# Performance work log

Hardware: AMD Instinct MI355X
Metric: run time of the kernel (lower is better)

The kernel has to match this reference:

```python
import jax, jax.numpy as jnp
import numpy as np

# (in_ch, out_ch) per conv layer per SA stage (use_xyz adds +3 to first in-ch)
DIMS = {1: [(3, 64), (64, 64), (64, 128)],
        2: [(131, 128), (128, 128), (128, 256)],
        3: [(259, 256), (256, 512), (512, 1024)]}
B, N = 32, 4096


def setup_inputs() -> dict:
    key = jax.random.key(0)
    key, k = jax.random.split(key)
    inp = {"pointcloud": jax.random.uniform(k, (B, N, 3), jnp.float32)}
    for s in (1, 2, 3):
        for l, (ci, co) in enumerate(DIMS[s]):
            key, k1, k2, k3 = jax.random.split(key, 4)
            inp[f"w{s}{l}"] = jax.random.normal(k1, (ci, co), jnp.float32) * (1.0 / np.sqrt(ci))
            # eval-mode BatchNorm folded to per-channel scale g and bias b
            inp[f"g{s}{l}"] = 1.0 + 0.1 * jax.random.normal(k2, (co,), jnp.float32)
            inp[f"b{s}{l}"] = 0.1 * jax.random.normal(k3, (co,), jnp.float32)
    return inp


def fps(xyz, npoint):
    """Farthest point sampling. xyz: (B,N,3) -> idx (B,npoint) int32. First index is 0."""
    n = xyz.shape[1]
    def one(pts):
        def body(carry, _):
            dist, last = carry
            d = jnp.sum((pts - pts[last]) ** 2, axis=-1)
            dist = jnp.minimum(dist, d)
            nxt = jnp.argmax(dist).astype(jnp.int32)
            return (dist, nxt), nxt
        init = (jnp.full((n,), 1e10, pts.dtype), jnp.int32(0))
        _, idxs = jax.lax.scan(body, init, None, length=npoint - 1)
        return jnp.concatenate([jnp.zeros((1,), jnp.int32), idxs])
    return jax.vmap(one)(xyz)


def ball_query(xyz, centers, radius, nsample):
    """xyz (B,N,3), centers (B,S,3) -> idx (B,S,nsample): first nsample in-ball point
    indices, deficits padded with the first found index (matches CUDA ball_query)."""
    n = xyz.shape[1]
    d2 = jnp.sum((centers[:, :, None, :] - xyz[:, None, :, :]) ** 2, axis=-1)  # (B,S,N)
    keyv = jnp.where(d2 < radius * radius, jnp.arange(n)[None, None, :], n)
    sk = jnp.sort(keyv, axis=-1)[..., :nsample]  # ascending valid indices, pad = n
    first = sk[..., :1]
    idx = jnp.where(sk == n, first, sk)
    return jnp.clip(idx, 0, n - 1)


def gather(pts, idx):
    """pts (B,N,C), idx (B,...) -> (B,...,C)"""
    return jax.vmap(lambda p, i: p[i])(pts, idx)


def shared_mlp(x, params):
    """x (..., Cin); each layer: 1x1 conv (matmul) + folded-BN affine + ReLU."""
    for w, g, b in params:
        x = jax.nn.relu(jnp.einsum('...c,cd->...d', x, w) * g + b)
    return x


def sa_module(xyz, feat, npoint, radius, nsample, params):
    ctr_idx = fps(xyz, npoint)
    new_xyz = gather(xyz, ctr_idx)                        # (B,S,3)
    idx = ball_query(xyz, new_xyz, radius, nsample)       # (B,S,K)
    g_xyz = gather(xyz, idx) - new_xyz[:, :, None, :]     # (B,S,K,3) centered
    grouped = g_xyz if feat is None else jnp.concatenate([g_xyz, gather(feat, idx)], axis=-1)
    h = shared_mlp(grouped, params)                       # (B,S,K,Cout)
    return new_xyz, jnp.max(h, axis=2)                    # max-pool over neighbors


def reference(pointcloud, w10, g10, b10, w11, g11, b11, w12, g12, b12,
              w20, g20, b20, w21, g21, b21, w22, g22, b22,
              w30, g30, b30, w31, g31, b31, w32, g32, b32):
    p1 = [(w10, g10, b10), (w11, g11, b11), (w12, g12, b12)]
    p2 = [(w20, g20, b20), (w21, g21, b21), (w22, g22, b22)]
    p3 = [(w30, g30, b30), (w31, g31, b31), (w32, g32, b32)]
    xyz = pointcloud[..., :3]
    xyz, feat = sa_module(xyz, None, 512, 0.2, 64, p1)
    xyz, feat = sa_module(xyz, feat, 128, 0.4, 64, p2)
    # group-all SA: one group containing all points, xyz NOT centered
    grouped = jnp.concatenate([xyz, feat], axis=-1)[:, None]  # (B,1,S,259)
    h = shared_mlp(grouped, p3)                                # (B,1,S,1024)
    return jnp.max(h, axis=2)[:, 0]                            # (B,1024)
```

## Files before the change

### kernel.cpp

```cpp
#include <hip/hip_runtime.h>
#include <math.h>

#define NTH 256

using short8 = __attribute__((ext_vector_type(8))) short;
using f32x4  = __attribute__((ext_vector_type(4))) float;

__device__ __forceinline__ unsigned short f2bf(float x) {
    unsigned u = __float_as_uint(x);
    u += 0x7fff + ((u >> 16) & 1);
    return (unsigned short)(u >> 16);
}
__device__ __forceinline__ float bf2f(unsigned short h) {
    return __uint_as_float(((unsigned)h) << 16);
}

template<int CTRL>
__device__ __forceinline__ unsigned long long dppmax(unsigned long long k) {
    unsigned lo = (unsigned)k, hi = (unsigned)(k >> 32);
    unsigned plo = (unsigned)__builtin_amdgcn_update_dpp(0, (int)lo, CTRL, 0xF, 0xF, true);
    unsigned phi = (unsigned)__builtin_amdgcn_update_dpp(0, (int)hi, CTRL, 0xF, 0xF, true);
    unsigned long long p = ((unsigned long long)phi << 32) | plo;
    return p > k ? p : k;
}

template<int N, int NPOINT, int NTHR, int NPC, bool INIT, bool SPILL>
__device__ __forceinline__ void fps_body(
    const float* __restrict__ xyz, float* __restrict__ out_xyz, int b, int it0,
    float* __restrict__ pts , float* __restrict__ ctr ,
    unsigned long long* __restrict__ wkey ,
    float* __restrict__ sdist, int* __restrict__ slast)
{
    constexpr int PT = N / NTHR;
    constexpr int NW = NTHR / 64;
    const int tid  = threadIdx.x;
    const int lane = tid & 63;
    const int w    = tid >> 6;
    const float* src = xyz + (size_t)b * N * 3;

    __builtin_amdgcn_s_setprio(1);

    for (int e = tid; e < N * 3; e += NTHR) pts[e] = src[e];

    float px[PT], py[PT], pz[PT], dist[PT];
    unsigned klo[PT];
#pragma unroll
    for (int j = 0; j < PT; ++j) {
        int i = j * NTHR + tid;
        px[j] = src[i * 3 + 0]; py[j] = src[i * 3 + 1]; pz[j] = src[i * 3 + 2];
        klo[j] = ~(unsigned)i;
        dist[j] = 1e10f;
    }
    int last = 0;
    if constexpr (!INIT) {
        const float* sd = sdist + (size_t)b * N;
#pragma unroll
        for (int j = 0; j < PT; ++j) dist[j] = sd[j * NTHR + tid];
        last = slast[b];
    } else {
        if (tid == 0) { ctr[0] = src[0]; ctr[1] = src[1]; ctr[2] = src[2]; }
    }
    __syncthreads();

    constexpr int CBEG = INIT ? 1 : 0;
    for (int c = CBEG; c < NPC; ++c) {
        const float lx = pts[last * 3 + 0];
        const float ly = pts[last * 3 + 1];
        const float lz = pts[last * 3 + 2];
        unsigned long long best = 0ull;
#pragma unroll
        for (int j = 0; j < PT; ++j) {
            float dx = px[j] - lx, dy = py[j] - ly, dz = pz[j] - lz;
            float d = __fadd_rn(__fadd_rn(__fmul_rn(dx, dx), __fmul_rn(dy, dy)),
                                __fmul_rn(dz, dz));
            float nd = fminf(dist[j], d);
            dist[j] = nd;
            unsigned long long key =
                ((unsigned long long)__float_as_uint(nd) << 32) | (unsigned long long)klo[j];
            best = (key > best) ? key : best;
        }
        best = dppmax<0xB1>(best);
        best = dppmax<0x4E>(best);
        best = dppmax<0x141>(best);
        best = dppmax<0x140>(best);
        best = dppmax<0x142>(best);
        best = dppmax<0x143>(best);
        const int p = (c & 1) * NW;
        if (lane == 63) wkey[p + w] = best;
        __syncthreads();
        unsigned long long K0[NW];
#pragma unroll
        for (int v = 0; v < NW; ++v) K0[v] = wkey[p + v];
#pragma unroll
        for (int st = NW / 2; st > 0; st >>= 1)
#pragma unroll
            for (int v = 0; v < st; ++v) K0[v] = (K0[v + st] > K0[v]) ? K0[v + st] : K0[v];
        last = (int)(~(unsigned)K0[0]);
        if (tid == 0) {
            ctr[c * 3 + 0] = pts[last * 3 + 0];
            ctr[c * 3 + 1] = pts[last * 3 + 1];
            ctr[c * 3 + 2] = pts[last * 3 + 2];
        }
    }
    __syncthreads();
    if constexpr (SPILL) {
        float* sd = sdist + (size_t)b * N;
#pragma unroll
        for (int j = 0; j < PT; ++j) sd[j * NTHR + tid] = dist[j];
        if (tid == 0) slast[b] = last;
    }
    float* dst = out_xyz + ((size_t)b * NPOINT + (it0 - CBEG)) * 3;
    for (int e = tid; e < NPC * 3; e += NTHR) dst[e] = ctr[e];
    __builtin_amdgcn_s_setprio(0);
}

#define PREP_TOT 813056
__device__ __forceinline__ void prep_body(
    int gid, int stride,
    const float* __restrict__ w0, const float* __restrict__ w1, const float* __restrict__ w2,
    const float* __restrict__ w3, const float* __restrict__ w4, const float* __restrict__ w5,
    const float* __restrict__ w6, const float* __restrict__ w7, const float* __restrict__ w8,
    unsigned short* __restrict__ outw)
{
    const int K_[9]    = {3, 64, 64, 131, 128, 128, 259, 256, 512};
    const int N_[9]    = {64, 64, 128, 128, 128, 256, 256, 512, 1024};
    const int E_[9]    = {2048, 4096, 8192, 20480, 16384, 32768, 73728, 131072, 524288};
    const int base_[9] = {0, 4096, 12288, 28672, 69632, 102400, 167936, 315392, 577536};
    const int PCF_[9]  = {0, 0, 0, 128, 0, 0, 256, 0, 0};
    const float* W_[9] = {w0, w1, w2, w3, w4, w5, w6, w7, w8};
    for (; gid < PREP_TOT; gid += stride) {
        int i = 0, t = gid;
        while (t >= E_[i]) { t -= E_[i]; ++i; }
        const int Nn = N_[i];
        const int k8 = t / (Nn * 8);
        const int rem = t - k8 * Nn * 8;
        const int col = rem >> 3, j = rem & 7;
        const int k = k8 * 8 + j;
        float v = 0.f;
        if (k < K_[i]) {
            int ks = k;
            const int pcf = PCF_[i];
            if (pcf > 0) ks = (k < pcf) ? (k + 3) : (k - pcf);
            v = W_[i][(size_t)ks * Nn + col];
        }
        unsigned short hi = f2bf(v);
        unsigned short lo = f2bf(v - bf2f(hi));
        outw[base_[i] + t] = hi;
        outw[base_[i] + E_[i] + t] = lo;
    }
}

template<int K, int NSUB, int NOFF, int NFULL, int RTILES, int SX, int SY, bool FINAL>
__device__ __forceinline__ void mfma_layer(
    const unsigned short* __restrict__ whi, const unsigned short* __restrict__ wlo,
    const float* __restrict__ gm, const float* __restrict__ bt,
    const unsigned short* __restrict__ Xhi, const unsigned short* __restrict__ Xlo,
    unsigned short* __restrict__ Yhi, unsigned short* __restrict__ Ylo,
    float* outp, int tid)
{
    constexpr int KP  = (K + 31) & ~31;
    constexpr int KC  = KP / 32;
    constexpr int NTW = NSUB / 64;
    static_assert(NSUB % 64 == 0, "col split");
    const int w = tid >> 6, lane = tid & 63;
    const int lr = lane & 15, lg = lane >> 4;
    const int colbase = NOFF + w * (NSUB / 4);

    f32x4 acc[RTILES][NTW];
#pragma unroll
    for (int m = 0; m < RTILES; ++m)
#pragma unroll
        for (int t = 0; t < NTW; ++t) acc[m][t] = f32x4{0.f, 0.f, 0.f, 0.f};

    const unsigned short* xh0 = Xhi + lr * SX + lg * 8;
    const unsigned short* xl0 = Xlo + lr * SX + lg * 8;

    for (int kc = 0; kc < KC; ++kc) {
        const size_t krow = (size_t)(kc * 4 + lg) * NFULL * 8;
        short8 bh[NTW], bl[NTW];
#pragma unroll
        for (int t = 0; t < NTW; ++t) {
            const int col = colbase + t * 16 + lr;
            bh[t] = *reinterpret_cast<const short8*>(whi + krow + (size_t)col * 8);
            bl[t] = *reinterpret_cast<const short8*>(wlo + krow + (size_t)col * 8);
        }
#pragma unroll
        for (int m = 0; m < RTILES; ++m) {
            short8 ah = *reinterpret_cast<const short8*>(xh0 + m * 16 * SX + kc * 32);
            short8 al = *reinterpret_cast<const short8*>(xl0 + m * 16 * SX + kc * 32);
#pragma unroll
            for (int t = 0; t < NTW; ++t) {
                acc[m][t] = __builtin_amdgcn_mfma_f32_16x16x32_bf16(ah, bh[t], acc[m][t], 0, 0, 0);
                acc[m][t] = __builtin_amdgcn_mfma_f32_16x16x32_bf16(ah, bl[t], acc[m][t], 0, 0, 0);
                acc[m][t] = __builtin_amdgcn_mfma_f32_16x16x32_bf16(al, bh[t], acc[m][t], 0, 0, 0);
            }
        }
    }
#pragma unroll
    for (int t = 0; t < NTW; ++t) {
        const int col = colbase + t * 16 + lr;
        const float gv = gm[col], bv = bt[col];
        if constexpr (FINAL) {
            float mx = 0.f;
#pragma unroll
            for (int m = 0; m < RTILES; ++m)
#pragma unroll
                for (int r = 0; r < 4; ++r)
                    mx = fmaxf(mx, fmaxf(fmaf(acc[m][t][r], gv, bv), 0.f));
            mx = fmaxf(mx, __shfl_xor(mx, 16));
            mx = fmaxf(mx, __shfl_xor(mx, 32));
            if (lg == 0)
                atomicMax(reinterpret_cast<int*>(outp) + col, __float_as_int(mx));
        } else {
#pragma unroll
            for (int m = 0; m < RTILES; ++m)
#pragma unroll
                for (int r = 0; r < 4; ++r) {
                    float v = fmaxf(fmaf(acc[m][t][r], gv, bv), 0.f);
                    unsigned short hi = f2bf(v);
                    unsigned short lo = f2bf(v - bf2f(hi));
                    const int row = m * 16 + lg * 4 + r;
                    Yhi[row * SY + col] = hi;
                    Ylo[row * SY + col] = lo;
                }
        }
    }
}

template<int CF, int C0, int C1, int C2, int R>
struct SaCfg {
    static constexpr int CIN = 3 + CF;
    static constexpr int KP0 = (CIN + 31) & ~31;
    static constexpr int SX = KP0 + 8, SY1 = C0 + 8, SY2 = C1 + 8;
    static constexpr int RT = R / 16;
    static constexpr int OFF_Y1 = 0;
    static constexpr int OFF_X = 2 * R * SY1;
    static constexpr int XSZ = 2 * R * SX, Y2SZ = 2 * R * SY2;
    static constexpr int TOT = OFF_X + (XSZ > Y2SZ ? XSZ : Y2SZ);
    static constexpr int BYTES = TOT * 2 + 264 * 4;
};

template<int CF, int C0, int C1, int C2, int R>
__device__ __forceinline__ void sa_body(
    unsigned short* __restrict__ sm, int* __restrict__ bqm,
    int b, int cs, int S, int half,
    const float* __restrict__ src_xyz, const float* __restrict__ src_feat,
    const float* __restrict__ centers,
    const unsigned short* __restrict__ w0h, const unsigned short* __restrict__ w0l,
    const unsigned short* __restrict__ w1h, const unsigned short* __restrict__ w1l,
    const unsigned short* __restrict__ w2h, const unsigned short* __restrict__ w2l,
    const float* __restrict__ g0, const float* __restrict__ b0,
    const float* __restrict__ g1, const float* __restrict__ b1,
    const float* __restrict__ g2, const float* __restrict__ b2,
    float* __restrict__ out_feat, int N, float r2)
{
    using C = SaCfg<CF, C0, C1, C2, R>;
    constexpr int TPR = NTH / R;
    const int tid  = threadIdx.x;
    const int lane = tid & 63;
    const int w    = tid >> 6;
    const int bs   = b * S + cs;

    const float cx = centers[(size_t)bs * 3 + 0];
    const float cy = centers[(size_t)bs * 3 + 1];
    const float cz = centers[(size_t)bs * 3 + 2];

    {
        const int seg = N >> 2;
        const float* px = src_xyz + (size_t)b * N * 3;
        int count = 0, first = -1;
        const int bend = (w + 1) * seg;
        for (int base = w * seg; base < bend && count < 64; base += 64) {
            int i = base + lane;
            float dx = px[i * 3 + 0] - cx, dy = px[i * 3 + 1] - cy, dz = px[i * 3 + 2] - cz;
            float d2 = __fadd_rn(__fadd_rn(__fmul_rn(dx, dx), __fmul_rn(dy, dy)),
                                 __fmul_rn(dz, dz));
            bool inb = d2 < r2;
            unsigned long long m = __ballot(inb);
            if (first < 0 && m) first = base + (__ffsll(m) - 1);
            if (inb) {
                int pos = count + (int)__popcll(m & ((1ull << lane) - 1ull));
                if (pos < 64) bqm[w * 64 + pos] = i;
            }
            count += (int)__popcll(m);
        }
        if (lane == 0) {
            bqm[256 + w] = count > 64 ? 64 : count;
            bqm[260 + w] = first;
        }
    }
    __syncthreads();

    unsigned short* Xhi = sm + C::OFF_X;    unsigned short* Xlo = Xhi + R * C::SX;
    unsigned short* Y1h = sm + C::OFF_Y1;   unsigned short* Y1l = Y1h + R * C::SY1;
    unsigned short* Y2h = sm + C::OFF_X;    unsigned short* Y2l = Y2h + R * C::SY2;

    {
        const int r = tid / TPR, s = tid % TPR;
        int pid;
        {
            const int cA = bqm[256 + 0], cB = bqm[256 + 1], cC = bqm[256 + 2], cD = bqm[256 + 3];
            const int tot = cA + cB + cC + cD;
            int t = half * R + r;
            if (t < tot) {
                int ww = 0;
                if (t >= cA) { t -= cA; ww = 1;
                    if (t >= cB) { t -= cB; ww = 2;
                        if (t >= cC) { t -= cC; ww = 3; } } }
                pid = bqm[ww * 64 + t];
            } else {
                const int fA = bqm[260 + 0], fB = bqm[260 + 1], fC = bqm[260 + 2], fD = bqm[260 + 3];
                pid = fA >= 0 ? fA : (fB >= 0 ? fB : (fC >= 0 ? fC : (fD >= 0 ? fD : (N - 1))));
            }
        }
        unsigned short* xh = Xhi + r * C::SX;
        unsigned short* xl = Xlo + r * C::SX;
        if constexpr (CF > 0) {
            constexpr int CPT = CF / TPR;
            const float* frow = src_feat + ((size_t)b * N + pid) * CF + s * CPT;
#pragma unroll
            for (int q = 0; q < CPT / 4; ++q) {
                float4 v4 = *reinterpret_cast<const float4*>(frow + q * 4);
                ushort4 h, l;
                h.x = f2bf(v4.x); l.x = f2bf(v4.x - bf2f(h.x));
                h.y = f2bf(v4.y); l.y = f2bf(v4.y - bf2f(h.y));
                h.z = f2bf(v4.z); l.z = f2bf(v4.z - bf2f(h.z));
                h.w = f2bf(v4.w); l.w = f2bf(v4.w - bf2f(h.w));
                *reinterpret_cast<ushort4*>(xh + s * CPT + q * 4) = h;
                *reinterpret_cast<ushort4*>(xl + s * CPT + q * 4) = l;
            }
        }
        if (s < 3) {
            float p = src_xyz[((size_t)b * N + pid) * 3 + s]
                      - (s == 0 ? cx : (s == 1 ? cy : cz));
            unsigned short hi = f2bf(p), lo = f2bf(p - bf2f(hi));
            xh[CF + s] = hi; xl[CF + s] = lo;
        }
        constexpr int PADPER = (C::KP0 - C::CIN + TPR - 1) / TPR;
#pragma unroll
        for (int q = 0; q < PADPER; ++q) {
            int c = C::CIN + s * PADPER + q;
            if (c < C::KP0) { xh[c] = 0; xl[c] = 0; }
        }
    }
    __syncthreads();
    mfma_layer<C::CIN, C0, 0, C0, C::RT, C::SX, C::SY1, false>(
        w0h, w0l, g0, b0, Xhi, Xlo, Y1h, Y1l, nullptr, tid);
    __syncthreads();
    mfma_layer<C0, C1, 0, C1, C::RT, C::SY1, C::SY2, false>(
        w1h, w1l, g1, b1, Y1h, Y1l, Y2h, Y2l, nullptr, tid);
    __syncthreads();
    mfma_layer<C1, C2, 0, C2, C::RT, C::SY2, 0, true>(
        w2h, w2l, g2, b2, Y2h, Y2l, nullptr, nullptr,
        out_feat + (size_t)bs * C2, tid);
}

template<int N1>
__global__ __launch_bounds__(NTH) void k_fps1a_prep(
    const float* __restrict__ pc, float* __restrict__ nxyz1,
    const float* __restrict__ w0, const float* __restrict__ w1, const float* __restrict__ w2,
    const float* __restrict__ w3, const float* __restrict__ w4, const float* __restrict__ w5,
    const float* __restrict__ w6, const float* __restrict__ w7, const float* __restrict__ w8,
    unsigned short* __restrict__ outw,
    float* __restrict__ sdist, int* __restrict__ slast,
    float4* __restrict__ z1, int n1, float4* __restrict__ z2, int n2,
    float4* __restrict__ z3, int n3, int nfps, int nprep)
{
    __shared__ float pts[N1 * 3];
    __shared__ float ctr[256 * 3];
    __shared__ unsigned long long wkey[2 * (NTH / 64)];
    if ((int)blockIdx.x < nfps) {
        fps_body<N1, 512, NTH, 256, true, true>(pc, nxyz1, blockIdx.x, 1,
                                                pts, ctr, wkey, sdist, slast);
    } else if ((int)blockIdx.x < nfps + nprep) {
        prep_body((blockIdx.x - nfps) * NTH + threadIdx.x, nprep * NTH,
                  w0, w1, w2, w3, w4, w5, w6, w7, w8, outw);
    } else {
        const int zid = (blockIdx.x - nfps - nprep) * NTH + threadIdx.x;
        const int zs  = (gridDim.x - nfps - nprep) * NTH;
        const float4 zv = make_float4(0.f, 0.f, 0.f, 0.f);
        for (int i = zid; i < n1; i += zs) z1[i] = zv;
        for (int i = zid; i < n2; i += zs) z2[i] = zv;
        for (int i = zid; i < n3; i += zs) z3[i] = zv;
    }
}

__global__ __launch_bounds__(NTH) void k_fps1b2_sa1h1(
    const float* __restrict__ pc, float* __restrict__ nxyz1, float* __restrict__ nxyz2,
    float* __restrict__ sdist, int* __restrict__ slast,
    const unsigned short* __restrict__ w0h, const unsigned short* __restrict__ w0l,
    const unsigned short* __restrict__ w1h, const unsigned short* __restrict__ w1l,
    const unsigned short* __restrict__ w2h, const unsigned short* __restrict__ w2l,
    const float* __restrict__ g0, const float* __restrict__ b0,
    const float* __restrict__ g1, const float* __restrict__ b1,
    const float* __restrict__ g2, const float* __restrict__ b2,
    float* __restrict__ feat1, float r2)
{
    constexpr int FPSB = 4096 * 3 * 4 + 256 * 3 * 4 + 2 * (NTH / 64) * 8;
    constexpr int SAB  = SaCfg<0, 64, 64, 128, 64>::BYTES;
    constexpr int BYTES = FPSB > SAB ? FPSB : SAB;
    __shared__ __align__(16) char raw[BYTES];
    if ((int)blockIdx.x < 32) {
        {
            float* pts = (float*)raw;
            float* ctr = (float*)(raw + 4096 * 3 * 4);
            unsigned long long* wkey = (unsigned long long*)(raw + 4096 * 3 * 4 + 256 * 3 * 4);
            fps_body<4096, 512, NTH, 256, false, false>(pc, nxyz1, blockIdx.x, 256,
                                                        pts, ctr, wkey, sdist, slast);
        }
        __syncthreads();
        {
            float* pts = (float*)raw;
            float* ctr = (float*)(raw + 512 * 3 * 4);
            unsigned long long* wkey = (unsigned long long*)(raw + 512 * 3 * 4 + 128 * 3 * 4);
            fps_body<512, 128, NTH, 128, true, false>(nxyz1, nxyz2, blockIdx.x, 1,
                                                      pts, ctr, wkey, nullptr, nullptr);
        }
    } else {
        const int blk = blockIdx.x - 32;
        const int b = blk >> 8, cs = blk & 255;
        unsigned short* sm = (unsigned short*)raw;
        int* bqm = (int*)(raw + SaCfg<0, 64, 64, 128, 64>::TOT * 2);
        sa_body<0, 64, 64, 128, 64>(sm, bqm, b, cs, 512, 0,
                                    pc, nullptr, nxyz1,
                                    w0h, w0l, w1h, w1l, w2h, w2l,
                                    g0, b0, g1, b1, g2, b2, feat1, 4096, r2);
    }
}

__global__ __launch_bounds__(NTH) void k_sa1h2(
    const float* __restrict__ pc, const float* __restrict__ nxyz1,
    const unsigned short* __restrict__ w0h, const unsigned short* __restrict__ w0l,
    const unsigned short* __restrict__ w1h, const unsigned short* __restrict__ w1l,
    const unsigned short* __restrict__ w2h, const unsigned short* __restrict__ w2l,
    const float* __restrict__ g0, const float* __restrict__ b0,
    const float* __restrict__ g1, const float* __restrict__ b1,
    const float* __restrict__ g2, const float* __restrict__ b2,
    float* __restrict__ feat1, float r2)
{
    using C = SaCfg<0, 64, 64, 128, 64>;
    __shared__ __align__(16) char raw[C::BYTES];
    const int b = blockIdx.x >> 8, cs = 256 + (blockIdx.x & 255);
    unsigned short* sm = (unsigned short*)raw;
    int* bqm = (int*)(raw + C::TOT * 2);
    sa_body<0, 64, 64, 128, 64>(sm, bqm, b, cs, 512, 0,
                                pc, nullptr, nxyz1,
                                w0h, w0l, w1h, w1l, w2h, w2l,
                                g0, b0, g1, b1, g2, b2, feat1, 4096, r2);
}

__global__ __launch_bounds__(NTH) void k_sa2(
    const float* __restrict__ nxyz1, const float* __restrict__ feat1,
    const float* __restrict__ nxyz2,
    const unsigned short* __restrict__ w0h, const unsigned short* __restrict__ w0l,
    const unsigned short* __restrict__ w1h, const unsigned short* __restrict__ w1l,
    const unsigned short* __restrict__ w2h, const unsigned short* __restrict__ w2l,
    const float* __restrict__ g0, const float* __restrict__ b0,
    const float* __restrict__ g1, const float* __restrict__ b1,
    const float* __restrict__ g2, const float* __restrict__ b2,
    float* __restrict__ feat2, float r2)
{
    using C = SaCfg<128, 128, 128, 256, 32>;
    __shared__ __align__(16) char raw[C::BYTES];
    const int half = blockIdx.x & 1;
    const int cb   = blockIdx.x >> 1;
    const int b = cb >> 7, cs = cb & 127;
    unsigned short* sm = (unsigned short*)raw;
    int* bqm = (int*)(raw + C::TOT * 2);
    sa_body<128, 128, 128, 256, 32>(sm, bqm, b, cs, 128, half,
                                    nxyz1, feat1, nxyz2,
                                    w0h, w0l, w1h, w1l, w2h, w2l,
                                    g0, b0, g1, b1, g2, b2, feat2, 512, r2);
}

template<int CF, int C0, int C1, int C2>
__global__ __launch_bounds__(NTH) void head_mfma(
    const float* __restrict__ xyz, const float* __restrict__ feat,
    const unsigned short* __restrict__ w0h, const unsigned short* __restrict__ w0l,
    const unsigned short* __restrict__ w1h, const unsigned short* __restrict__ w1l,
    const unsigned short* __restrict__ w2h, const unsigned short* __restrict__ w2l,
    const float* __restrict__ g0, const float* __restrict__ b0,
    const float* __restrict__ g1, const float* __restrict__ b1,
    const float* __restrict__ g2, const float* __restrict__ b2,
    float* __restrict__ out, int Np)
{
    constexpr int R = 16;
    constexpr int CIN = 3 + CF;
    constexpr int KP0 = (CIN + 31) & ~31;
    constexpr int SX = KP0 + 8, SY1 = C0 + 8, SY2 = C1 + 8;
    constexpr int OFF_Y1 = 0;
    constexpr int OFF_X  = 2 * R * SY1;
    constexpr int XSZ = 2 * R * SX, Y2SZ = 2 * R * SY2;
    constexpr int TOT = OFF_X + (XSZ > Y2SZ ? XSZ : Y2SZ);
    __shared__ __align__(16) unsigned short sm[TOT];
    constexpr int TPR = NTH / R;

    const int tid = threadIdx.x;
    const int chunks = Np / R;
    const int b  = blockIdx.x / chunks;
    const int r0 = (blockIdx.x % chunks) * R;

    unsigned short* Xhi = sm + OFF_X;   unsigned short* Xlo = Xhi + R * SX;
    unsigned short* Y1h = sm + OFF_Y1;  unsigned short* Y1l = Y1h + R * SY1;
    unsigned short* Y2h = sm + OFF_X;   unsigned short* Y2l = Y2h + R * SY2;

    {
        const int r = tid / TPR, s = tid % TPR;
        const int row = r0 + r;
        unsigned short* xh = Xhi + r * SX;
        unsigned short* xl = Xlo + r * SX;
        constexpr int CPT = CF / TPR;
        const float* frow = feat + ((size_t)b * Np + row) * CF + s * CPT;
#pragma unroll
        for (int q = 0; q < CPT / 4; ++q) {
            float4 v4 = *reinterpret_cast<const float4*>(frow + q * 4);
            ushort4 h, l;
            h.x = f2bf(v4.x); l.x = f2bf(v4.x - bf2f(h.x));
            h.y = f2bf(v4.y); l.y = f2bf(v4.y - bf2f(h.y));
            h.z = f2bf(v4.z); l.z = f2bf(v4.z - bf2f(h.z));
            h.w = f2bf(v4.w); l.w = f2bf(v4.w - bf2f(h.w));
            *reinterpret_cast<ushort4*>(xh + s * CPT + q * 4) = h;
            *reinterpret_cast<ushort4*>(xl + s * CPT + q * 4) = l;
        }
        if (s < 3) {
            float p = xyz[((size_t)b * Np + row) * 3 + s];
            unsigned short hi = f2bf(p), lo = f2bf(p - bf2f(hi));
            xh[CF + s] = hi; xl[CF + s] = lo;
        }
        constexpr int PADPER = (KP0 - CIN + TPR - 1) / TPR;
#pragma unroll
        for (int q = 0; q < PADPER; ++q) {
            int c = CIN + s * PADPER + q;
            if (c < KP0) { xh[c] = 0; xl[c] = 0; }
        }
    }
    __syncthreads();
    mfma_layer<CIN, C0, 0, C0, 1, SX, SY1, false>(w0h, w0l, g0, b0, Xhi, Xlo, Y1h, Y1l, nullptr, tid);
    __syncthreads();
    mfma_layer<C0, C1, 0, C1, 1, SY1, SY2, false>(w1h, w1l, g1, b1, Y1h, Y1l, Y2h, Y2l, nullptr, tid);
    __syncthreads();
    float* op = out + (size_t)b * C2;
    mfma_layer<C1, C2 / 2, 0,      C2, 1, SY2, 0, true>(w2h, w2l, g2, b2, Y2h, Y2l, nullptr, nullptr, op, tid);
    mfma_layer<C1, C2 / 2, C2 / 2, C2, 1, SY2, 0, true>(w2h, w2l, g2, b2, Y2h, Y2l, nullptr, nullptr, op, tid);
}

extern "C" void kernel_launch(void* const* d_in, const int* in_sizes, int n_in,
                              void* d_out, int out_size, void* d_ws, size_t ws_size,
                              hipStream_t stream)
{
    (void)in_sizes; (void)n_in; (void)ws_size;
    const int B = 32;
    const float* pc = (const float*)d_in[0];
    const float* W[27];
    for (int i = 0; i < 27; ++i) W[i] = (const float*)d_in[1 + i];
    float* out = (float*)d_out;

    char* ws = (char*)d_ws;
    size_t off = 0;
    auto take = [&](size_t bytes) {
        void* p = ws + off;
        off += (bytes + 255) & ~(size_t)255;
        return p;
    };
    float* nxyz1 = (float*)take((size_t)B * 512 * 3 * 4);
    float* feat1 = (float*)take((size_t)B * 512 * 128 * 4);
    float* nxyz2 = (float*)take((size_t)B * 128 * 3 * 4);
    float* feat2 = (float*)take((size_t)B * 128 * 256 * 4);
    unsigned short* wf = (unsigned short*)take((size_t)1626112 * 2);
    float* sdist = (float*)take((size_t)B * 4096 * 4);
    int*   slast = (int*)take((size_t)B * 4);

    const int E_[9]    = {2048, 4096, 8192, 20480, 16384, 32768, 73728, 131072, 524288};
    const int base_[9] = {0, 4096, 12288, 28672, 69632, 102400, 167936, 315392, 577536};
    const unsigned short* wh[9]; const unsigned short* wl[9];
    for (int i = 0; i < 9; ++i) { wh[i] = wf + base_[i]; wl[i] = wf + base_[i] + E_[i]; }

    const float r2_1 = (float)(0.2 * 0.2);
    const float r2_2 = (float)(0.4 * 0.4);

    k_fps1a_prep<4096><<<32 + 512 + 64, NTH, 0, stream>>>(
        pc, nxyz1,
        W[0], W[3], W[6], W[9], W[12], W[15], W[18], W[21], W[24],
        wf, sdist, slast,
        (float4*)feat1, B * 512 * 128 / 4,
        (float4*)feat2, B * 128 * 256 / 4,
        (float4*)out,   out_size / 4,
        32, 512);

    k_fps1b2_sa1h1<<<32 + B * 256, NTH, 0, stream>>>(
        pc, nxyz1, nxyz2, sdist, slast,
        wh[0], wl[0], wh[1], wl[1], wh[2], wl[2],
        W[1], W[2], W[4], W[5], W[7], W[8],
        feat1, r2_1);

    k_sa1h2<<<B * 256, NTH, 0, stream>>>(
        pc, nxyz1,
        wh[0], wl[0], wh[1], wl[1], wh[2], wl[2],
        W[1], W[2], W[4], W[5], W[7], W[8],
        feat1, r2_1);

    k_sa2<<<B * 128 * 2, NTH, 0, stream>>>(
        nxyz1, feat1, nxyz2,
        wh[3], wl[3], wh[4], wl[4], wh[5], wl[5],
        W[10], W[11], W[13], W[14], W[16], W[17],
        feat2, r2_2);

    head_mfma<256, 256, 512, 1024><<<B * 8, NTH, 0, stream>>>(
        nxyz2, feat2,
        wh[6], wl[6], wh[7], wl[7], wh[8], wl[8],
        W[19], W[20], W[22], W[23], W[25], W[26],
        out, 128);
}
```

Measured before the change: 649.6 us.

## Move stage-2 FPS into second SA1 kernel as single-wave DPP reduction

```diff
diff --git a/kernel.cpp b/kernel.cpp
--- a/kernel.cpp
+++ b/kernel.cpp
@@ -112,6 +112,67 @@
     float* dst = out_xyz + ((size_t)b * NPOINT + (it0 - CBEG)) * 3;
     for (int e = tid; e < NPC * 3; e += NTHR) dst[e] = ctr[e];
     __builtin_amdgcn_s_setprio(0);
+}
+
+template<int N, int NPOINT>
+__device__ __forceinline__ void fps2_wave_body(
+    const float* __restrict__ xyz, float* __restrict__ out_xyz, int b,
+    float* __restrict__ pts , float* __restrict__ ctr )
+{
+    const int tid = threadIdx.x;
+    const float* src = xyz + (size_t)b * N * 3;
+    for (int e = tid; e < N * 3; e += NTH) pts[e] = src[e];
+    __syncthreads();
+    if (tid < 64) {
+        __builtin_amdgcn_s_setprio(1);
+        constexpr int PT = N / 64;
+        const int lane = tid;
+        float px[PT], py[PT], pz[PT], dist[PT];
+        unsigned klo[PT];
+#pragma unroll
+        for (int j = 0; j < PT; ++j) {
+            int i = j * 64 + lane;
+            px[j] = pts[i * 3 + 0]; py[j] = pts[i * 3 + 1]; pz[j] = pts[i * 3 + 2];
+            dist[j] = 1e10f;
+            klo[j] = ~(unsigned)i;
+        }
+        int last = 0;
+        if (lane == 0) { ctr[0] = pts[0]; ctr[1] = pts[1]; ctr[2] = pts[2]; }
+        for (int it = 1; it < NPOINT; ++it) {
+            const float lx = pts[last * 3 + 0];
+            const float ly = pts[last * 3 + 1];
+            const float lz = pts[last * 3 + 2];
+            unsigned long long best = 0ull;
+#pragma unroll
+            for (int j = 0; j < PT; ++j) {
+                float dx = px[j] - lx, dy = py[j] - ly, dz = pz[j] - lz;
+                float d = __fadd_rn(__fadd_rn(__fmul_rn(dx, dx), __fmul_rn(dy, dy)),
+                                    __fmul_rn(dz, dz));
+                float nd = fminf(dist[j], d);
+                dist[j] = nd;
+                unsigned long long key =
+                    ((unsigned long long)__float_as_uint(nd) << 32) | (unsigned long long)klo[j];
+                best = (key > best) ? key : best;
+            }
+            best = dppmax<0xB1>(best);
+            best = dppmax<0x4E>(best);
+            best = dppmax<0x141>(best);
+            best = dppmax<0x140>(best);
+            best = dppmax<0x142>(best);
+            best = dppmax<0x143>(best);
+            unsigned long long g = __shfl(best, 63);
+            last = (int)(~(unsigned)g);
+            if (lane == 0) {
+                ctr[it * 3 + 0] = pts[last * 3 + 0];
+                ctr[it * 3 + 1] = pts[last * 3 + 1];
+                ctr[it * 3 + 2] = pts[last * 3 + 2];
+            }
+        }
+        __builtin_amdgcn_s_setprio(0);
+    }
+    __syncthreads();
+    float* dst = out_xyz + (size_t)b * NPOINT * 3;
+    for (int e = tid; e < NPOINT * 3; e += NTH) dst[e] = ctr[e];
 }
 
 #define PREP_TOT 813056
@@ -385,8 +446,8 @@
     }
 }
 
-__global__ __launch_bounds__(NTH) void k_fps1b2_sa1h1(
-    const float* __restrict__ pc, float* __restrict__ nxyz1, float* __restrict__ nxyz2,
+__global__ __launch_bounds__(NTH) void k_fps1b_sa1h1(
+    const float* __restrict__ pc, float* __restrict__ nxyz1,
     float* __restrict__ sdist, int* __restrict__ slast,
     const unsigned short* __restrict__ w0h, const unsigned short* __restrict__ w0l,
     const unsigned short* __restrict__ w1h, const unsigned short* __restrict__ w1l,
@@ -401,21 +462,11 @@
     constexpr int BYTES = FPSB > SAB ? FPSB : SAB;
     __shared__ __align__(16) char raw[BYTES];
     if ((int)blockIdx.x < 32) {
-        {
-            float* pts = (float*)raw;
-            float* ctr = (float*)(raw + 4096 * 3 * 4);
-            unsigned long long* wkey = (unsigned long long*)(raw + 4096 * 3 * 4 + 256 * 3 * 4);
-            fps_body<4096, 512, NTH, 256, false, false>(pc, nxyz1, blockIdx.x, 256,
-                                                        pts, ctr, wkey, sdist, slast);
-        }
-        __syncthreads();
-        {
-            float* pts = (float*)raw;
-            float* ctr = (float*)(raw + 512 * 3 * 4);
-            unsigned long long* wkey = (unsigned long long*)(raw + 512 * 3 * 4 + 128 * 3 * 4);
-            fps_body<512, 128, NTH, 128, true, false>(nxyz1, nxyz2, blockIdx.x, 1,
-                                                      pts, ctr, wkey, nullptr, nullptr);
-        }
+        float* pts = (float*)raw;
+        float* ctr = (float*)(raw + 4096 * 3 * 4);
+        unsigned long long* wkey = (unsigned long long*)(raw + 4096 * 3 * 4 + 256 * 3 * 4);
+        fps_body<4096, 512, NTH, 256, false, false>(pc, nxyz1, blockIdx.x, 256,
+                                                    pts, ctr, wkey, sdist, slast);
     } else {
         const int blk = blockIdx.x - 32;
         const int b = blk >> 8, cs = blk & 255;
@@ -428,8 +479,9 @@
     }
 }
 
-__global__ __launch_bounds__(NTH) void k_sa1h2(
+__global__ __launch_bounds__(NTH) void k_fps2_sa1h2(
     const float* __restrict__ pc, const float* __restrict__ nxyz1,
+    float* __restrict__ nxyz2,
     const unsigned short* __restrict__ w0h, const unsigned short* __restrict__ w0l,
     const unsigned short* __restrict__ w1h, const unsigned short* __restrict__ w1l,
     const unsigned short* __restrict__ w2h, const unsigned short* __restrict__ w2l,
@@ -438,15 +490,24 @@
     const float* __restrict__ g2, const float* __restrict__ b2,
     float* __restrict__ feat1, float r2)
 {
-    using C = SaCfg<0, 64, 64, 128, 64>;
-    __shared__ __align__(16) char raw[C::BYTES];
-    const int b = blockIdx.x >> 8, cs = 256 + (blockIdx.x & 255);
-    unsigned short* sm = (unsigned short*)raw;
-    int* bqm = (int*)(raw + C::TOT * 2);
-    sa_body<0, 64, 64, 128, 64>(sm, bqm, b, cs, 512, 0,
-                                pc, nullptr, nxyz1,
-                                w0h, w0l, w1h, w1l, w2h, w2l,
-                                g0, b0, g1, b1, g2, b2, feat1, 4096, r2);
+    constexpr int FPSB = 512 * 3 * 4 + 128 * 3 * 4;
+    constexpr int SAB  = SaCfg<0, 64, 64, 128, 64>::BYTES;
+    constexpr int BYTES = FPSB > SAB ? FPSB : SAB;
+    __shared__ __align__(16) char raw[BYTES];
+    if ((int)blockIdx.x < 32) {
+        float* pts = (float*)raw;
+        float* ctr = (float*)(raw + 512 * 3 * 4);
+        fps2_wave_body<512, 128>(nxyz1, nxyz2, blockIdx.x, pts, ctr);
+    } else {
+        const int blk = blockIdx.x - 32;
+        const int b = blk >> 8, cs = 256 + (blk & 255);
+        unsigned short* sm = (unsigned short*)raw;
+        int* bqm = (int*)(raw + SaCfg<0, 64, 64, 128, 64>::TOT * 2);
+        sa_body<0, 64, 64, 128, 64>(sm, bqm, b, cs, 512, 0,
+                                    pc, nullptr, nxyz1,
+                                    w0h, w0l, w1h, w1l, w2h, w2l,
+                                    g0, b0, g1, b1, g2, b2, feat1, 4096, r2);
+    }
 }
 
 __global__ __launch_bounds__(NTH) void k_sa2(
@@ -587,14 +648,14 @@
         (float4*)out,   out_size / 4,
         32, 512);
 
-    k_fps1b2_sa1h1<<<32 + B * 256, NTH, 0, stream>>>(
-        pc, nxyz1, nxyz2, sdist, slast,
+    k_fps1b_sa1h1<<<32 + B * 256, NTH, 0, stream>>>(
+        pc, nxyz1, sdist, slast,
         wh[0], wl[0], wh[1], wl[1], wh[2], wl[2],
         W[1], W[2], W[4], W[5], W[7], W[8],
         feat1, r2_1);
 
-    k_sa1h2<<<B * 256, NTH, 0, stream>>>(
-        pc, nxyz1,
+    k_fps2_sa1h2<<<32 + B * 256, NTH, 0, stream>>>(
+        pc, nxyz1, nxyz2,
         wh[0], wl[0], wh[1], wl[1], wh[2], wl[2],
         W[1], W[2], W[4], W[5], W[7], W[8],
         feat1, r2_1);
```

Result: faster. 607.4 us (-6.5%).
